# Kernel optimization log

Measured on AMD Instinct MI355X. Metric: run time of the kernel, lower is better.

The kernel has to match this reference:

```python
import jax, jax.numpy as jnp
import numpy as np

K, T, F = 12000, 35, 7          # voxels, points-per-voxel (cfg.VOXEL_POINT_COUNT), point feature dim
B, D, H, W = 1, 10, 400, 352    # scatter grid: [batch, depth, cfg.INPUT_HEIGHT, cfg.INPUT_WIDTH]
C_OUT = 128
EPS = 1e-3                      # Keras BatchNormalization default epsilon


def setup_inputs() -> dict:
    key = jax.random.key(0)
    ks = jax.random.split(key, 20)
    # point features, with per-voxel padding (points beyond count are zero)
    feat = jax.random.normal(ks[0], (K, T, F), dtype=jnp.float32)
    counts = jax.random.randint(ks[1], (K,), 1, T + 1)
    valid = (jnp.arange(T)[None, :] < counts[:, None]).astype(jnp.float32)  # [K,T]
    feat = feat * valid[:, :, None]
    # voxel coordinates: (batch, d, h, w), in-range per dimension
    c0 = jax.random.randint(ks[2], (K,), 0, B)
    c1 = jax.random.randint(ks[3], (K,), 0, D)
    c2 = jax.random.randint(ks[4], (K,), 0, H)
    c3 = jax.random.randint(ks[5], (K,), 0, W)
    coordinate = jnp.stack([c0, c1, c2, c3], axis=1).astype(jnp.int32)  # [K,4]
    p = lambda i, shape: jax.random.normal(ks[i], shape, dtype=jnp.float32) * 0.1
    return {
        "input_feature": feat,
        "w1": p(6, (F, 16)), "b1": p(7, (16,)),
        "gamma1": 1.0 + p(8, (16,)), "beta1": p(9, (16,)),
        "mean1": p(10, (16,)), "var1": jax.random.uniform(ks[11], (16,), minval=0.5, maxval=1.5),
        "w2": p(12, (32, 64)), "b2": p(13, (64,)),
        "gamma2": 1.0 + p(14, (64,)), "beta2": p(15, (64,)),
        "mean2": p(16, (64,)), "var2": jax.random.uniform(ks[17], (64,), minval=0.5, maxval=1.5),
        "coordinate": coordinate,
        "batch_size": B,
    }


def vfe(x, mask, w, b, gamma, beta, mean, var):
    # Dense + relu (per point), inference BatchNorm, max-aggregate, tile-concat, mask
    dense = jax.nn.relu(jnp.einsum('ktf,fu->ktu', x, w) + b)
    pw = gamma * (dense - mean) * jax.lax.rsqrt(var + EPS) + beta  # [K,T,U]
    agg = jnp.max(pw, axis=1, keepdims=True)                       # [K,1,U]
    cat = jnp.concatenate([pw, jnp.broadcast_to(agg, pw.shape)], axis=2)  # [K,T,2U]
    return cat * mask


def reference(input_feature, w1, b1, gamma1, beta1, mean1, var1,
              w2, b2, gamma2, beta2, mean2, var2, coordinate, batch_size):
    # mask: point is valid if max over its features != 0
    mask = (jnp.max(input_feature, axis=2, keepdims=True) != 0).astype(input_feature.dtype)
    x = vfe(input_feature, mask, w1, b1, gamma1, beta1, mean1, var1)   # [K,T,32]
    x = vfe(x, mask, w2, b2, gamma2, beta2, mean2, var2)               # [K,T,128]
    voxelwise = jnp.max(x, axis=1)                                     # [K,128]
    out = jnp.zeros((batch_size, D, H, W, C_OUT), dtype=voxelwise.dtype)
    # tf.scatter_nd semantics: duplicate indices accumulate (add)
    out = out.at[coordinate[:, 0], coordinate[:, 1], coordinate[:, 2], coordinate[:, 3]].add(voxelwise)
    return out
```

## Files before the change

kernel.cpp:

```cpp
#include <hip/hip_runtime.h>

#define KVOX 12000
#define TPTS 35
#define FIN  7
#define DD   10
#define HH   400
#define WW   352
#define CO   128
#define EPSBN 1e-3f
#define NCELL (DD * HH * WW)
#define CB    3000
#define TOTALF4 ((size_t)NCELL * 32)
#define SB    1500

static_assert(CB * 4 == KVOX, "grid covers voxels exactly");

__global__ __launch_bounds__(256) void fused_fill_compute(
    const float* __restrict__ feat,
    const float* __restrict__ w1, const float* __restrict__ b1,
    const float* __restrict__ g1, const float* __restrict__ be1,
    const float* __restrict__ m1, const float* __restrict__ v1,
    const float* __restrict__ w2, const float* __restrict__ b2,
    const float* __restrict__ g2, const float* __restrict__ be2,
    const float* __restrict__ m2, const float* __restrict__ v2,
    float* __restrict__ vox,
    float* __restrict__ out)
{
    const int tid  = threadIdx.x;
    const int wv   = tid >> 6;
    const int lane = tid & 63;
    const int k    = blockIdx.x * 4 + wv;

    __shared__ __align__(16) float sxp[4][TPTS][8];
    __shared__ __align__(16) float spwm[4][TPTS][16];
    __shared__ __align__(16) float sagg[4][16];

    const bool fillFirst = (blockIdx.x & 1);

    auto do_fill = [&]() {
        const float4 z = make_float4(0.f, 0.f, 0.f, 0.f);
        float4* o4 = (float4*)out;
        const size_t stride = (size_t)CB * 256;
        for (size_t i = (size_t)blockIdx.x * 256 + tid; i < TOTALF4; i += stride)
            o4[i] = z;
    };

    if (fillFirst) do_fill();

    const float* fk = feat + (size_t)k * (TPTS * FIN);

    for (int i = lane; i < TPTS * FIN; i += 64)
        sxp[wv][i / FIN][i % FIN] = fk[i];
    if (lane < TPTS) sxp[wv][lane][FIN] = 0.0f;

    bool pred = false;
    if (lane < TPTS) {
        const float* row = fk + lane * FIN;
        float mx = row[0];
        #pragma unroll
        for (int f = 1; f < FIN; ++f) mx = fmaxf(mx, row[f]);
        pred = (mx != 0.0f);
    }
    const unsigned long long bal = __ballot(pred);
    const int nvalid = __popcll(bal);
    __syncthreads();

    if (lane < 16) {
        const int u = lane;
        float w1c[8];
        #pragma unroll
        for (int f = 0; f < FIN; ++f) w1c[f] = w1[f * 16 + u];
        w1c[FIN] = 0.0f;
        const float b     = b1[u];
        const float scale = g1[u] * rsqrtf(v1[u] + EPSBN);
        const float shift = be1[u] - m1[u] * scale;

        float agg = -INFINITY;
        float pw[TPTS];
        #pragma unroll
        for (int t = 0; t < TPTS; ++t) {
            const float4 xa = *(const float4*)&sxp[wv][t][0];
            const float4 xb = *(const float4*)&sxp[wv][t][4];
            float d = b;
            d = fmaf(xa.x, w1c[0], d); d = fmaf(xa.y, w1c[1], d);
            d = fmaf(xa.z, w1c[2], d); d = fmaf(xa.w, w1c[3], d);
            d = fmaf(xb.x, w1c[4], d); d = fmaf(xb.y, w1c[5], d);
            d = fmaf(xb.z, w1c[6], d); d = fmaf(xb.w, w1c[7], d);
            d = fmaxf(d, 0.0f);
            const float p = fmaf(d, scale, shift);
            agg = fmaxf(agg, p);
            pw[t] = p;
        }
        sagg[wv][u] = agg;
        #pragma unroll
        for (int t = 0; t < TPTS; ++t) {
            const float mk = ((bal >> t) & 1ULL) ? 1.0f : 0.0f;
            spwm[wv][t][u] = pw[t] * mk;
        }
    }
    __syncthreads();

    {
        const int v = lane;
        float w2c[32];
        #pragma unroll
        for (int u = 0; u < 32; ++u) w2c[u] = w2[u * 64 + v];
        const float b     = b2[v];
        const float scale = g2[v] * rsqrtf(v2[v] + EPSBN);
        const float shift = be2[v] - m2[v] * scale;

        float aggdot = 0.0f;
        {
            const float4* ar = (const float4*)&sagg[wv][0];
            #pragma unroll
            for (int q = 0; q < 4; ++q) {
                const float4 a = ar[q];
                aggdot = fmaf(a.x, w2c[16 + 4 * q + 0], aggdot);
                aggdot = fmaf(a.y, w2c[16 + 4 * q + 1], aggdot);
                aggdot = fmaf(a.z, w2c[16 + 4 * q + 2], aggdot);
                aggdot = fmaf(a.w, w2c[16 + 4 * q + 3], aggdot);
            }
        }

        float aggAll = -INFINITY;
        float voxA   = -INFINITY;
        #pragma unroll 7
        for (int t = 0; t < TPTS; ++t) {
            const float mk = ((bal >> t) & 1ULL) ? 1.0f : 0.0f;
            const float4* xr = (const float4*)&spwm[wv][t][0];
            float d = fmaf(mk, aggdot, b);
            #pragma unroll
            for (int q = 0; q < 4; ++q) {
                const float4 xv = xr[q];
                d = fmaf(xv.x, w2c[4 * q + 0], d);
                d = fmaf(xv.y, w2c[4 * q + 1], d);
                d = fmaf(xv.z, w2c[4 * q + 2], d);
                d = fmaf(xv.w, w2c[4 * q + 3], d);
            }
            d = fmaxf(d, 0.0f);
            const float p = fmaf(d, scale, shift);
            aggAll = fmaxf(aggAll, p);
            voxA   = fmaxf(voxA, p * mk);
        }
        float voxB;
        if (nvalid == 0)          voxB = 0.0f;
        else if (nvalid < TPTS)   voxB = fmaxf(aggAll, 0.0f);
        else                      voxB = aggAll;

        float* vk = vox + (size_t)k * CO;
        vk[v]      = voxA;
        vk[64 + v] = voxB;
    }

    if (!fillFirst) do_fill();
}

__global__ __launch_bounds__(256) void scatter_add(
    const float* __restrict__ vox, const int* __restrict__ coord,
    float* __restrict__ out)
{
    const int stride = SB * 256;
    for (int i = blockIdx.x * 256 + threadIdx.x; i < KVOX * CO; i += stride) {
        const int k  = i >> 7;
        const int ch = i & (CO - 1);
        const int4 c = ((const int4*)coord)[k];
        const int loc = (((c.x * DD + c.y) * HH + c.z) * WW + c.w);
        atomicAdd(out + (size_t)loc * CO + ch, vox[i]);
    }
}

__global__ __launch_bounds__(64) void vfe_scatter_atomic(
    const float* __restrict__ feat,
    const float* __restrict__ w1, const float* __restrict__ b1,
    const float* __restrict__ g1, const float* __restrict__ be1,
    const float* __restrict__ m1, const float* __restrict__ v1,
    const float* __restrict__ w2, const float* __restrict__ b2,
    const float* __restrict__ g2, const float* __restrict__ be2,
    const float* __restrict__ m2, const float* __restrict__ v2,
    const int* __restrict__ coord,
    float* __restrict__ out)
{
    const int k   = blockIdx.x;
    const int tid = threadIdx.x;
    __shared__ float sx[TPTS][FIN];
    __shared__ float smask[TPTS];
    __shared__ __align__(16) float sx2[TPTS][32];
    const float* fk = feat + (size_t)k * (TPTS * FIN);
    for (int i = tid; i < TPTS * FIN; i += 64) ((float*)sx)[i] = fk[i];
    __syncthreads();
    bool pred = false;
    if (tid < TPTS) {
        float mx = sx[tid][0];
        #pragma unroll
        for (int f = 1; f < FIN; ++f) mx = fmaxf(mx, sx[tid][f]);
        pred = (mx != 0.0f);
        smask[tid] = pred ? 1.0f : 0.0f;
    }
    unsigned long long bal = __ballot(pred);
    const int nvalid = __popcll(bal);
    __syncthreads();
    if (tid < 16) {
        const int u = tid;
        float w1c[FIN];
        #pragma unroll
        for (int f = 0; f < FIN; ++f) w1c[f] = w1[f * 16 + u];
        const float b = b1[u];
        const float scale = g1[u] * rsqrtf(v1[u] + EPSBN);
        const float shift = be1[u] - m1[u] * scale;
        float agg = -INFINITY;
        float pw[TPTS];
        #pragma unroll
        for (int t = 0; t < TPTS; ++t) {
            float d = b;
            #pragma unroll
            for (int f = 0; f < FIN; ++f) d = fmaf(sx[t][f], w1c[f], d);
            d = fmaxf(d, 0.0f);
            float p = fmaf(d, scale, shift);
            agg = fmaxf(agg, p);
            pw[t] = p;
        }
        #pragma unroll
        for (int t = 0; t < TPTS; ++t) {
            const float mk = smask[t];
            sx2[t][u] = pw[t] * mk;
            sx2[t][16 + u] = agg * mk;
        }
    }
    __syncthreads();
    {
        const int v = tid;
        float w2c[32];
        #pragma unroll
        for (int u = 0; u < 32; ++u) w2c[u] = w2[u * 64 + v];
        const float b = b2[v];
        const float scale = g2[v] * rsqrtf(v2[v] + EPSBN);
        const float shift = be2[v] - m2[v] * scale;
        float aggAll = -INFINITY, voxA = -INFINITY;
        #pragma unroll 5
        for (int t = 0; t < TPTS; ++t) {
            float d = b;
            const float4* xr = (const float4*)(&sx2[t][0]);
            #pragma unroll
            for (int q = 0; q < 8; ++q) {
                float4 xv = xr[q];
                d = fmaf(xv.x, w2c[4 * q + 0], d);
                d = fmaf(xv.y, w2c[4 * q + 1], d);
                d = fmaf(xv.z, w2c[4 * q + 2], d);
                d = fmaf(xv.w, w2c[4 * q + 3], d);
            }
            d = fmaxf(d, 0.0f);
            float p = fmaf(d, scale, shift);
            aggAll = fmaxf(aggAll, p);
            voxA = fmaxf(voxA, p * smask[t]);
        }
        float voxB;
        if (nvalid == 0) voxB = 0.0f;
        else if (nvalid < TPTS) voxB = fmaxf(aggAll, 0.0f);
        else voxB = aggAll;
        const int4 c = ((const int4*)coord)[k];
        const int loc = (((c.x * DD + c.y) * HH + c.z) * WW + c.w);
        float* o = out + (size_t)loc * CO;
        atomicAdd(o + v, voxA);
        atomicAdd(o + 64 + v, voxB);
    }
}

extern "C" void kernel_launch(void* const* d_in, const int* in_sizes, int n_in,
                              void* d_out, int out_size, void* d_ws, size_t ws_size,
                              hipStream_t stream) {
    const float* feat = (const float*)d_in[0];
    const float* w1   = (const float*)d_in[1];
    const float* b1   = (const float*)d_in[2];
    const float* g1   = (const float*)d_in[3];
    const float* be1  = (const float*)d_in[4];
    const float* m1   = (const float*)d_in[5];
    const float* v1   = (const float*)d_in[6];
    const float* w2   = (const float*)d_in[7];
    const float* b2   = (const float*)d_in[8];
    const float* g2   = (const float*)d_in[9];
    const float* be2  = (const float*)d_in[10];
    const float* m2   = (const float*)d_in[11];
    const float* v2   = (const float*)d_in[12];
    const int*   coord = (const int*)d_in[13];
    float* out = (float*)d_out;

    const size_t voxB = (size_t)KVOX * CO * sizeof(float);

    if (ws_size >= voxB) {
        float* vox = (float*)d_ws;
        fused_fill_compute<<<CB, 256, 0, stream>>>(feat, w1, b1, g1, be1, m1, v1,
                                                   w2, b2, g2, be2, m2, v2,
                                                   vox, out);
        scatter_add<<<SB, 256, 0, stream>>>(vox, coord, out);
    } else {
        hipMemsetAsync(d_out, 0, (size_t)out_size * sizeof(float), stream);
        vfe_scatter_atomic<<<KVOX, 64, 0, stream>>>(feat, w1, b1, g1, be1, m1, v1,
                                                    w2, b2, g2, be2, m2, v2, coord, out);
    }
}
```

Measured before the change: 751.3 us.

## Split output zero-fill into contiguous per-block chunks interleaved with compute phases

The zero-fill of the large output grid now gives each block a contiguous chunk instead of a grid-strided range. The stores are issued in three slices around the VFE compute phases, so memory writes overlap with the arithmetic. The scatter kernel also loads vox as float4 and issues four atomics per thread, which cuts index math and load instructions. Contiguous chunks could change DRAM access patterns, and the fixed 20-iteration slices assume a particular chunk size.

```diff
diff --git a/kernel.cpp b/kernel.cpp
--- a/kernel.cpp
+++ b/kernel.cpp
@@ -11,6 +11,7 @@
 #define NCELL (DD * HH * WW)
 #define CB    3000
 #define TOTALF4 ((size_t)NCELL * 32)
+#define F4_PER_BLK 15019
 #define SB    1500
 
 static_assert(CB * 4 == KVOX, "grid covers voxels exactly");
@@ -35,20 +36,16 @@
     __shared__ __align__(16) float spwm[4][TPTS][16];
     __shared__ __align__(16) float sagg[4][16];
 
-    const bool fillFirst = (blockIdx.x & 1);
-
-    auto do_fill = [&]() {
-        const float4 z = make_float4(0.f, 0.f, 0.f, 0.f);
-        float4* o4 = (float4*)out;
-        const size_t stride = (size_t)CB * 256;
-        for (size_t i = (size_t)blockIdx.x * 256 + tid; i < TOTALF4; i += stride)
-            o4[i] = z;
-    };
-
-    if (fillFirst) do_fill();
+    const float4 z = make_float4(0.f, 0.f, 0.f, 0.f);
+    float4* o4 = (float4*)out;
+    const size_t chunk_end = min((size_t)(blockIdx.x + 1) * F4_PER_BLK, TOTALF4);
+    size_t fi = (size_t)blockIdx.x * F4_PER_BLK + tid;
+
+    #pragma unroll 4
+    for (int it = 0; it < 20; ++it, fi += 256)
+        if (fi < chunk_end) o4[fi] = z;
 
     const float* fk = feat + (size_t)k * (TPTS * FIN);
-
     for (int i = lane; i < TPTS * FIN; i += 64)
         sxp[wv][i / FIN][i % FIN] = fk[i];
     if (lane < TPTS) sxp[wv][lane][FIN] = 0.0f;
@@ -64,6 +61,10 @@
     const unsigned long long bal = __ballot(pred);
     const int nvalid = __popcll(bal);
     __syncthreads();
+
+    #pragma unroll 4
+    for (int it = 0; it < 20; ++it, fi += 256)
+        if (fi < chunk_end) o4[fi] = z;
 
     if (lane < 16) {
         const int u = lane;
@@ -99,6 +100,9 @@
         }
     }
     __syncthreads();
+
+    for (; fi < chunk_end; fi += 256)
+        o4[fi] = z;
 
     {
         const int v = lane;
@@ -151,21 +155,25 @@
         vk[v]      = voxA;
         vk[64 + v] = voxB;
     }
-
-    if (!fillFirst) do_fill();
 }
 
 __global__ __launch_bounds__(256) void scatter_add(
     const float* __restrict__ vox, const int* __restrict__ coord,
     float* __restrict__ out)
 {
+    const int nquad = KVOX * (CO / 4);
     const int stride = SB * 256;
-    for (int i = blockIdx.x * 256 + threadIdx.x; i < KVOX * CO; i += stride) {
-        const int k  = i >> 7;
-        const int ch = i & (CO - 1);
+    for (int i = blockIdx.x * 256 + threadIdx.x; i < nquad; i += stride) {
+        const int k = i >> 5;
+        const int q = (i & 31) << 2;
         const int4 c = ((const int4*)coord)[k];
         const int loc = (((c.x * DD + c.y) * HH + c.z) * WW + c.w);
-        atomicAdd(out + (size_t)loc * CO + ch, vox[i]);
+        const float4 v = ((const float4*)vox)[i];
+        float* o = out + (size_t)loc * CO + q;
+        atomicAdd(o + 0, v.x);
+        atomicAdd(o + 1, v.y);
+        atomicAdd(o + 2, v.z);
+        atomicAdd(o + 3, v.w);
     }
 }
 
```

New measurement: 789.6 us. 1.05x slower.

## Contiguous per-block zero-fill chunks, wave-level LDS fences, and hoisted weight loads

Applied to the files above, without the earlier changes.

The output zero-fill is rewritten so each block clears one contiguous chunk of float4s instead of a grid-strided interleave. The fill now sits between feature staging and compute, replacing the alternating fill-first/fill-last ordering. Block-wide __syncthreads are replaced by per-wave waitcnt plus wave barriers, since each wave only touches its own LDS slice. Weight and BatchNorm parameter loads are hoisted to kernel entry so their latency overlaps other work. This trades coalesced cross-block striding for sequential per-block streams and uses more registers early in the kernel.

```diff
diff --git a/kernel.cpp b/kernel.cpp
--- a/kernel.cpp
+++ b/kernel.cpp
@@ -9,11 +9,18 @@
 #define CO   128
 #define EPSBN 1e-3f
 #define NCELL (DD * HH * WW)
+#define TOTALF4 ((size_t)NCELL * 32)
 #define CB    3000
-#define TOTALF4 ((size_t)NCELL * 32)
+#define F4PB  15019
 #define SB    1500
 
 static_assert(CB * 4 == KVOX, "grid covers voxels exactly");
+static_assert((size_t)CB * F4PB >= TOTALF4, "fill chunks cover output");
+
+__device__ __forceinline__ void wave_lds_fence() {
+    asm volatile("s_waitcnt lgkmcnt(0)" ::: "memory");
+    __builtin_amdgcn_wave_barrier();
+}
 
 __global__ __launch_bounds__(256) void fused_fill_compute(
     const float* __restrict__ feat,
@@ -35,20 +42,25 @@
     __shared__ __align__(16) float spwm[4][TPTS][16];
     __shared__ __align__(16) float sagg[4][16];
 
-    const bool fillFirst = (blockIdx.x & 1);
-
-    auto do_fill = [&]() {
-        const float4 z = make_float4(0.f, 0.f, 0.f, 0.f);
-        float4* o4 = (float4*)out;
-        const size_t stride = (size_t)CB * 256;
-        for (size_t i = (size_t)blockIdx.x * 256 + tid; i < TOTALF4; i += stride)
-            o4[i] = z;
-    };
-
-    if (fillFirst) do_fill();
+    float w2c[32];
+    #pragma unroll
+    for (int u = 0; u < 32; ++u) w2c[u] = w2[u * 64 + lane];
+    const float b2v    = b2[lane];
+    const float scale2 = g2[lane] * rsqrtf(v2[lane] + EPSBN);
+    const float shift2 = be2[lane] - m2[lane] * scale2;
+
+    float w1c[8];
+    float b1v = 0.f, scale1 = 0.f, shift1 = 0.f;
+    if (lane < 16) {
+        #pragma unroll
+        for (int f = 0; f < FIN; ++f) w1c[f] = w1[f * 16 + lane];
+        w1c[FIN] = 0.0f;
+        b1v    = b1[lane];
+        scale1 = g1[lane] * rsqrtf(v1[lane] + EPSBN);
+        shift1 = be1[lane] - m1[lane] * scale1;
+    }
 
     const float* fk = feat + (size_t)k * (TPTS * FIN);
-
     for (int i = lane; i < TPTS * FIN; i += 64)
         sxp[wv][i / FIN][i % FIN] = fk[i];
     if (lane < TPTS) sxp[wv][lane][FIN] = 0.0f;
@@ -63,31 +75,34 @@
     }
     const unsigned long long bal = __ballot(pred);
     const int nvalid = __popcll(bal);
-    __syncthreads();
+
+    asm volatile("s_waitcnt vmcnt(0) lgkmcnt(0)" ::: "memory");
+    __builtin_amdgcn_wave_barrier();
+
+    {
+        const float4 z = make_float4(0.f, 0.f, 0.f, 0.f);
+        float4* o4 = (float4*)out;
+        const size_t base = (size_t)blockIdx.x * F4PB;
+        const size_t end  = min(base + F4PB, TOTALF4);
+        for (size_t i = base + tid; i < end; i += 256)
+            o4[i] = z;
+    }
 
     if (lane < 16) {
         const int u = lane;
-        float w1c[8];
-        #pragma unroll
-        for (int f = 0; f < FIN; ++f) w1c[f] = w1[f * 16 + u];
-        w1c[FIN] = 0.0f;
-        const float b     = b1[u];
-        const float scale = g1[u] * rsqrtf(v1[u] + EPSBN);
-        const float shift = be1[u] - m1[u] * scale;
-
         float agg = -INFINITY;
         float pw[TPTS];
         #pragma unroll
         for (int t = 0; t < TPTS; ++t) {
             const float4 xa = *(const float4*)&sxp[wv][t][0];
             const float4 xb = *(const float4*)&sxp[wv][t][4];
-            float d = b;
+            float d = b1v;
             d = fmaf(xa.x, w1c[0], d); d = fmaf(xa.y, w1c[1], d);
             d = fmaf(xa.z, w1c[2], d); d = fmaf(xa.w, w1c[3], d);
             d = fmaf(xb.x, w1c[4], d); d = fmaf(xb.y, w1c[5], d);
             d = fmaf(xb.z, w1c[6], d); d = fmaf(xb.w, w1c[7], d);
             d = fmaxf(d, 0.0f);
-            const float p = fmaf(d, scale, shift);
+            const float p = fmaf(d, scale1, shift1);
             agg = fmaxf(agg, p);
             pw[t] = p;
         }
@@ -98,17 +113,10 @@
             spwm[wv][t][u] = pw[t] * mk;
         }
     }
-    __syncthreads();
+    wave_lds_fence();
 
     {
         const int v = lane;
-        float w2c[32];
-        #pragma unroll
-        for (int u = 0; u < 32; ++u) w2c[u] = w2[u * 64 + v];
-        const float b     = b2[v];
-        const float scale = g2[v] * rsqrtf(v2[v] + EPSBN);
-        const float shift = be2[v] - m2[v] * scale;
-
         float aggdot = 0.0f;
         {
             const float4* ar = (const float4*)&sagg[wv][0];
@@ -128,7 +136,7 @@
         for (int t = 0; t < TPTS; ++t) {
             const float mk = ((bal >> t) & 1ULL) ? 1.0f : 0.0f;
             const float4* xr = (const float4*)&spwm[wv][t][0];
-            float d = fmaf(mk, aggdot, b);
+            float d = fmaf(mk, aggdot, b2v);
             #pragma unroll
             for (int q = 0; q < 4; ++q) {
                 const float4 xv = xr[q];
@@ -138,7 +146,7 @@
                 d = fmaf(xv.w, w2c[4 * q + 3], d);
             }
             d = fmaxf(d, 0.0f);
-            const float p = fmaf(d, scale, shift);
+            const float p = fmaf(d, scale2, shift2);
             aggAll = fmaxf(aggAll, p);
             voxA   = fmaxf(voxA, p * mk);
         }
@@ -151,8 +159,6 @@
         vk[v]      = voxA;
         vk[64 + v] = voxB;
     }
-
-    if (!fillFirst) do_fill();
 }
 
 __global__ __launch_bounds__(256) void scatter_add(
```

New measurement: 771.4 us. 1.03x slower.
